# Optimization experiments

Measured on AMD Instinct MI355X. Metric: run time of the kernel, lower is better.

Reference implementation:

```python
import jax, jax.numpy as jnp
import numpy as np

B, T, C, H = 8, 1024, 1024, 16
HD = C // H  # head dim = 64
NEG = -1e9


def setup_inputs() -> dict:
    key = jax.random.key(0)
    ks = jax.random.split(key, 10)
    total = B * T
    x = jax.random.normal(ks[0], (total, C), dtype=jnp.float32)
    # identity pack: each padded row is a contiguous chunk of tokens
    padpack_index = jnp.arange(total, dtype=jnp.int64).reshape(B, T)
    # sorted per-row sequence ids -> block-diagonal attention within each packed row
    padpack_batch = jnp.sort(jax.random.randint(ks[1], (B, T), 0, 4, dtype=jnp.int32), axis=-1)
    padpack_inverse_index = jnp.arange(total, dtype=jnp.int64)
    s = 1.0 / np.sqrt(C)
    Wq = jax.random.uniform(ks[2], (C, C), jnp.float32, -s, s)
    bq = jax.random.uniform(ks[3], (C,), jnp.float32, -s, s)
    Wk = jax.random.uniform(ks[4], (C, C), jnp.float32, -s, s)
    bk = jax.random.uniform(ks[5], (C,), jnp.float32, -s, s)
    Wv = jax.random.uniform(ks[6], (C, C), jnp.float32, -s, s)
    bv = jax.random.uniform(ks[7], (C,), jnp.float32, -s, s)
    Wp = jax.random.uniform(ks[8], (C, C), jnp.float32, -s, s)
    bp = jax.random.uniform(ks[9], (C,), jnp.float32, -s, s)
    return {"x": x, "padpack_index": padpack_index, "padpack_batch": padpack_batch,
            "padpack_inverse_index": padpack_inverse_index,
            "Wq": Wq, "bq": bq, "Wk": Wk, "bk": bk, "Wv": Wv, "bv": bv, "Wp": Wp, "bp": bp}


def reference(x, padpack_index, padpack_batch, padpack_inverse_index,
              Wq, bq, Wk, bk, Wv, bv, Wp, bp):
    # gather ragged tokens into padded [B, T, C]
    xp = x[padpack_index]
    # torch Linear: y = x @ W.T + b
    q = (xp @ Wq.T + bq).reshape(B, T, H, HD)
    k = (xp @ Wk.T + bk).reshape(B, T, H, HD)
    v = (xp @ Wv.T + bv).reshape(B, T, H, HD)
    scale = 1.0 / np.sqrt(HD).astype(np.float32)
    att = jnp.einsum('bihd,bjhd->bhij', q, k) * scale  # [B,H,T,T]
    # mask: token pairs from different packed sequences cannot attend
    mask = (padpack_batch[:, :, None] != padpack_batch[:, None, :])[:, None]  # [B,1,T,T]
    att = jnp.where(mask, NEG, att)
    att = jax.nn.softmax(att, axis=-1)
    y = jnp.einsum('bhij,bjhd->bihd', att, v).reshape(B, T, C)
    y = y @ Wp.T + bp
    # scatter back to ragged layout [total_tokens, C]
    return y.reshape(B * T, C)[padpack_inverse_index]
```

## Files before the change

### kernel.cpp

```cpp
#include <hip/hip_runtime.h>


typedef __attribute__((ext_vector_type(8))) short short8;
typedef __attribute__((ext_vector_type(4))) float f32x4;

#define MFMA16(a, b, c) __builtin_amdgcn_mfma_f32_16x16x32_bf16((a), (b), (c), 0, 0, 0)

__device__ __forceinline__ ushort f2b(float f) {
  union { float f; unsigned u; } v; v.f = f;
  unsigned u = v.u;
  return (ushort)((u + 0x7fffu + ((u >> 16) & 1u)) >> 16);
}

__device__ __forceinline__ void gload16(const void* g, void* l) {
  __builtin_amdgcn_global_load_lds((const __attribute__((address_space(1))) unsigned int*)g,
                                   (__attribute__((address_space(3))) unsigned int*)l,
                                   16, 0, 0);
}

__device__ __forceinline__ void cvt4(const float* __restrict__ s, ushort* __restrict__ d) {
  const float4 v = *(const float4*)s;
  ushort4 r; r.x = f2b(v.x); r.y = f2b(v.y); r.z = f2b(v.z); r.w = f2b(v.w);
  *(ushort4*)d = r;
}

__global__ __launch_bounds__(256) void prep(const float* __restrict__ x,
    const float* __restrict__ wq, const float* __restrict__ wk,
    const float* __restrict__ wv, const float* __restrict__ wp,
    ushort* __restrict__ xb, ushort* __restrict__ wb) {
  const long long e0 = ((long long)blockIdx.x * 256 + threadIdx.x) * 4;
  const long long NX = 8388608ll;
  if (e0 < NX) {
    cvt4(x + e0, xb + e0);
  } else {
    const long long t = e0 - NX;
    const int sel = (int)(t >> 20);
    const float* w = sel == 0 ? wq : sel == 1 ? wk : sel == 2 ? wv : wp;
    cvt4(w + (t & 1048575), wb + t);
  }
}

__global__ void seg_bounds(const int* __restrict__ pb, int* __restrict__ bnd) {
  const int b = blockIdx.x, i = threadIdx.x;
  const int* p = pb + b * 1024;
  const int cur = p[i];
  const int prev = (i == 0) ? -1 : p[i - 1];
  for (int v = prev + 1; v <= cur; ++v) bnd[b * 8 + v] = i;
  if (i == 1023)
    for (int v = cur + 1; v <= 4; ++v) bnd[b * 8 + v] = 1024;
}

__global__ __launch_bounds__(256) void gemm_qkv(const ushort* __restrict__ X,
    const ushort* __restrict__ Wq, const ushort* __restrict__ Wk, const ushort* __restrict__ Wv,
    const float* __restrict__ bq, const float* __restrict__ bk, const float* __restrict__ bv,
    ushort* __restrict__ Qb, ushort* __restrict__ Kb, ushort* __restrict__ Vt) {
  __shared__ __align__(16) char smem[33792];
  ushort (*As)[32] = (ushort(*)[32])smem;
  ushort (*Bs)[32] = (ushort(*)[32])(smem + 8192);

  const int z = blockIdx.z;
  const ushort* W = (z == 0) ? Wq : (z == 1) ? Wk : Wv;
  const float* bias = (z == 0) ? bq : (z == 1) ? bk : bv;

  const int tid = threadIdx.x;
  const int lane = tid & 63, wv4 = tid >> 6;
  const int wr = wv4 >> 1, wc = wv4 & 1;
  const int lg = lane >> 4, lc = lane & 15;
  const int m0 = blockIdx.y * 128, n0 = blockIdx.x * 128;

  f32x4 acc[4][4] = {};

  const ushort* ga = X + (size_t)(m0 + (tid >> 2)) * 1024 + (tid & 3) * 8;
  const ushort* gb = W + (size_t)(n0 + (tid >> 2)) * 1024 + (tid & 3) * 8;
  char* la = smem + tid * 16;
  char* lb = smem + 8192 + tid * 16;

  for (int k0 = 0; k0 < 1024; k0 += 32) {
    gload16(ga + k0, la);
    gload16(ga + k0 + 64 * 1024, la + 4096);
    gload16(gb + k0, lb);
    gload16(gb + k0 + 64 * 1024, lb + 4096);
    __syncthreads();
    short8 af[4], bfr[4];
#pragma unroll
    for (int m = 0; m < 4; ++m) af[m] = *(const short8*)&As[wr * 64 + m * 16 + lc][lg * 8];
#pragma unroll
    for (int n = 0; n < 4; ++n) bfr[n] = *(const short8*)&Bs[wc * 64 + n * 16 + lc][lg * 8];
#pragma unroll
    for (int m = 0; m < 4; ++m)
#pragma unroll
      for (int n = 0; n < 4; ++n)
        acc[m][n] = MFMA16(af[m], bfr[n], acc[m][n]);
    __syncthreads();
  }

  float bval[4];
#pragma unroll
  for (int n = 0; n < 4; ++n) bval[n] = bias[n0 + wc * 64 + n * 16 + lc];

  if (z < 2) {
    ushort* dst = z ? Kb : Qb;
#pragma unroll
    for (int m = 0; m < 4; ++m)
#pragma unroll
      for (int j = 0; j < 4; ++j) {
        const size_t row = m0 + wr * 64 + m * 16 + lg * 4 + j;
#pragma unroll
        for (int n = 0; n < 4; ++n)
          dst[row * 1024 + n0 + wc * 64 + n * 16 + lc] = f2b(acc[m][n][j] + bval[n]);
      }
  } else {
    ushort (*Ts)[132] = (ushort(*)[132])smem;
#pragma unroll
    for (int m = 0; m < 4; ++m)
#pragma unroll
      for (int n = 0; n < 4; ++n)
#pragma unroll
        for (int j = 0; j < 4; ++j)
          Ts[wr * 64 + m * 16 + lg * 4 + j][wc * 64 + n * 16 + lc] = f2b(acc[m][n][j] + bval[n]);
    __syncthreads();
    const int c = tid >> 1;
    const int th = (tid & 1) * 64;
    const int gc = n0 + c;
    const int gt = m0 + th;
    const int b = gt >> 10, t = gt & 1023;
    ushort* dp = Vt + ((size_t)((b * 16 + (gc >> 6)) * 64 + (gc & 63))) * 1024 + t;
#pragma unroll
    for (int g = 0; g < 8; ++g) {
      short8 pk;
#pragma unroll
      for (int u = 0; u < 8; ++u) pk[u] = (short)Ts[th + g * 8 + u][c];
      *(short8*)(dp + g * 8) = pk;
    }
  }
}

__global__ __launch_bounds__(256) void attn(const ushort* __restrict__ Q,
    const ushort* __restrict__ K, const ushort* __restrict__ Vt,
    const int* __restrict__ bnd, ushort* __restrict__ O) {
  __shared__ __align__(16) char kvbuf[2][16384];
  __shared__ __align__(16) ushort Plds[4][16][68];

  const int tid = threadIdx.x, lane = tid & 63, w = tid >> 6;
  const int lg = lane >> 4, lc = lane & 15;

  const int id = blockIdx.x;
  const int xcd = id & 7, slot = id >> 3;
  const int bh = xcd + 8 * (slot >> 4), qt = slot & 15;
  const int b = bh >> 4, h = bh & 15;
  const int q0 = qt * 64 + w * 16;

  const int* bd = bnd + b * 8;
  const int b1 = bd[1], b2 = bd[2], b3 = bd[3], b4 = bd[4];
#define SEGID(k) (((k) >= b1) + ((k) >= b2) + ((k) >= b3) + ((k) >= b4))

  const int qid = SEGID(q0 + lc);
  int klo_l = (qid > 0) ? b1 : 0;
  klo_l = (qid > 1) ? b2 : klo_l;
  klo_l = (qid > 2) ? b3 : klo_l;
  int khi_l = (qid > 0) ? b2 : b1;
  khi_l = (qid > 1) ? b3 : khi_l;
  khi_l = (qid > 2) ? b4 : khi_l;

  const int bq_lo = SEGID(qt * 64), bq_hi = SEGID(qt * 64 + 63);
  unsigned am = 0;
#pragma unroll
  for (int jt = 0; jt < 16; ++jt) {
    const int tlo = SEGID(jt * 64), thi = SEGID(jt * 64 + 63);
    if (thi >= bq_lo && tlo <= bq_hi) am |= (1u << jt);
  }

  const ushort* qp = Q + (size_t)(b * 1024 + q0 + lc) * 1024 + h * 64 + lg * 8;
  const short8 qf0 = *(const short8*)qp;
  const short8 qf1 = *(const short8*)(qp + 32);

  const int r0 = tid >> 3;
  const int c16 = (tid & 7) ^ (r0 & 7);
  const ushort* Kg0 = K + (size_t)(b * 1024 + r0) * 1024 + h * 64 + c16 * 8;
  const ushort* Kg1 = Kg0 + (size_t)32 * 1024;
  const ushort* Vg0 = Vt + (size_t)(bh * 64 + r0) * 1024 + c16 * 8;
  const ushort* Vg1 = Vg0 + (size_t)32 * 1024;

#define STAGE(bufp, j) { \
    gload16(Kg0 + (size_t)(j) * 1024, (bufp) + tid * 16); \
    gload16(Kg1 + (size_t)(j) * 1024, (bufp) + 4096 + tid * 16); \
    gload16(Vg0 + (j), (bufp) + 8192 + tid * 16); \
    gload16(Vg1 + (j), (bufp) + 12288 + tid * 16); }

#define SOFF(r, ch) ((r) * 128 + ((((ch) ^ ((r) & 7))) << 4))

  float mr = -1e30f, lr = 0.f;
  f32x4 o[4] = {};

  unsigned rem = am;
  int jc = __builtin_ctz(rem) * 64;
  rem &= rem - 1;
  STAGE(kvbuf[0], jc)
  __syncthreads();
  int cur = 0;

  for (;;) {
    int jn = -1;
    if (rem) {
      jn = __builtin_ctz(rem) * 64;
      rem &= rem - 1;
      STAGE(kvbuf[cur ^ 1], jn)
    }
    const char* bufK = kvbuf[cur];
    const char* bufV = kvbuf[cur] + 8192;

    short8 kf[8];
#pragma unroll
    for (int n = 0; n < 4; ++n) {
      const int rr = n * 16 + lc;
      kf[2 * n] = *(const short8*)(bufK + SOFF(rr, lg));
      kf[2 * n + 1] = *(const short8*)(bufK + SOFF(rr, lg + 4));
    }
    f32x4 s[4];
    __builtin_amdgcn_s_setprio(1);
#pragma unroll
    for (int n = 0; n < 4; ++n) {
      f32x4 z = {};
      z = MFMA16(kf[2 * n], qf0, z);
      s[n] = MFMA16(kf[2 * n + 1], qf1, z);
    }
    __builtin_amdgcn_s_setprio(0);

#pragma unroll
    for (int n = 0; n < 4; ++n) {
      const int kk = jc + n * 16 + lg * 4;
#pragma unroll
      for (int r = 0; r < 4; ++r) {
        const bool ok = (kk + r >= klo_l) && (kk + r < khi_l);
        s[n][r] = ok ? s[n][r] * 0.125f : -1e9f;
      }
    }

    float rm = fmaxf(fmaxf(fmaxf(s[0][0], s[0][1]), fmaxf(s[0][2], s[0][3])),
                     fmaxf(fmaxf(fmaxf(s[1][0], s[1][1]), fmaxf(s[1][2], s[1][3])),
                           fmaxf(fmaxf(fmaxf(s[2][0], s[2][1]), fmaxf(s[2][2], s[2][3])),
                                 fmaxf(fmaxf(s[3][0], s[3][1]), fmaxf(s[3][2], s[3][3])))));
    rm = fmaxf(rm, __shfl_xor(rm, 16));
    rm = fmaxf(rm, __shfl_xor(rm, 32));
    float mn = mr;
    if (!__all(rm <= mr + 8.f)) {
      mn = fmaxf(mr, rm);
      const float sf = __expf(mr - mn);
      mr = mn;
      lr *= sf;
      const float s0 = __shfl(sf, lg * 4 + 0);
      const float s1 = __shfl(sf, lg * 4 + 1);
      const float s2 = __shfl(sf, lg * 4 + 2);
      const float s3 = __shfl(sf, lg * 4 + 3);
#pragma unroll
      for (int n = 0; n < 4; ++n) {
        o[n][0] *= s0; o[n][1] *= s1; o[n][2] *= s2; o[n][3] *= s3;
      }
    }
    float rs = 0.f;
#pragma unroll
    for (int n = 0; n < 4; ++n)
#pragma unroll
      for (int r = 0; r < 4; ++r) {
        const float p = __expf(s[n][r] - mn);
        s[n][r] = p; rs += p;
      }
    rs += __shfl_xor(rs, 16);
    rs += __shfl_xor(rs, 32);
    lr += rs;

#pragma unroll
    for (int n = 0; n < 4; ++n) {
      ushort4 pk;
      pk.x = f2b(s[n][0]); pk.y = f2b(s[n][1]); pk.z = f2b(s[n][2]); pk.w = f2b(s[n][3]);
      *(ushort4*)&Plds[w][lc][n * 16 + lg * 4] = pk;
    }
    asm volatile("s_waitcnt lgkmcnt(0)" ::: "memory");
    __builtin_amdgcn_sched_barrier(0);
    const short8 p0 = *(const short8*)&Plds[w][lc][lg * 8];
    const short8 p1 = *(const short8*)&Plds[w][lc][32 + lg * 8];
    __builtin_amdgcn_sched_barrier(0);

    short8 vv[8];
#pragma unroll
    for (int n = 0; n < 4; ++n) {
      const int rr = n * 16 + lc;
      vv[2 * n] = *(const short8*)(bufV + SOFF(rr, lg));
      vv[2 * n + 1] = *(const short8*)(bufV + SOFF(rr, lg + 4));
    }
    __builtin_amdgcn_s_setprio(1);
#pragma unroll
    for (int n = 0; n < 4; ++n) {
      o[n] = MFMA16(p0, vv[2 * n], o[n]);
      o[n] = MFMA16(p1, vv[2 * n + 1], o[n]);
    }
    __builtin_amdgcn_s_setprio(0);

    if (jn < 0) break;
    __syncthreads();
    cur ^= 1;
    jc = jn;
  }

  const float linv = 1.f / lr;
  const float i0 = __shfl(linv, lg * 4 + 0);
  const float i1 = __shfl(linv, lg * 4 + 1);
  const float i2 = __shfl(linv, lg * 4 + 2);
  const float i3 = __shfl(linv, lg * 4 + 3);
#pragma unroll
  for (int n = 0; n < 4; ++n) {
    const size_t base = (size_t)(b * 1024 + q0) * 1024 + h * 64 + n * 16 + lc;
    O[base + 0 * 1024 + (size_t)lg * 4096] = f2b(o[n][0] * i0);
    O[base + 1 * 1024 + (size_t)lg * 4096] = f2b(o[n][1] * i1);
    O[base + 2 * 1024 + (size_t)lg * 4096] = f2b(o[n][2] * i2);
    O[base + 3 * 1024 + (size_t)lg * 4096] = f2b(o[n][3] * i3);
  }
#undef STAGE
#undef SOFF
#undef SEGID
}

__global__ __launch_bounds__(256) void gemm_proj(const ushort* __restrict__ X,
    const ushort* __restrict__ W, const float* __restrict__ bias, float* __restrict__ out) {
  __shared__ __align__(16) char smem[16384];
  ushort (*As)[32] = (ushort(*)[32])smem;
  ushort (*Bs)[32] = (ushort(*)[32])(smem + 8192);
  const int tid = threadIdx.x;
  const int lane = tid & 63, wv4 = tid >> 6;
  const int wr = wv4 >> 1, wc = wv4 & 1;
  const int lg = lane >> 4, lc = lane & 15;
  const int m0 = blockIdx.y * 128, n0 = blockIdx.x * 128;
  f32x4 acc[4][4] = {};
  const ushort* ga = X + (size_t)(m0 + (tid >> 2)) * 1024 + (tid & 3) * 8;
  const ushort* gb = W + (size_t)(n0 + (tid >> 2)) * 1024 + (tid & 3) * 8;
  char* la = smem + tid * 16;
  char* lb = smem + 8192 + tid * 16;
  for (int k0 = 0; k0 < 1024; k0 += 32) {
    gload16(ga + k0, la);
    gload16(ga + k0 + 64 * 1024, la + 4096);
    gload16(gb + k0, lb);
    gload16(gb + k0 + 64 * 1024, lb + 4096);
    __syncthreads();
    short8 af[4], bfr[4];
#pragma unroll
    for (int m = 0; m < 4; ++m) af[m] = *(const short8*)&As[wr * 64 + m * 16 + lc][lg * 8];
#pragma unroll
    for (int n = 0; n < 4; ++n) bfr[n] = *(const short8*)&Bs[wc * 64 + n * 16 + lc][lg * 8];
#pragma unroll
    for (int m = 0; m < 4; ++m)
#pragma unroll
      for (int n = 0; n < 4; ++n)
        acc[m][n] = MFMA16(af[m], bfr[n], acc[m][n]);
    __syncthreads();
  }
  float bval[4];
#pragma unroll
  for (int n = 0; n < 4; ++n) bval[n] = bias[n0 + wc * 64 + n * 16 + lc];
#pragma unroll
  for (int m = 0; m < 4; ++m)
#pragma unroll
    for (int j = 0; j < 4; ++j) {
      const size_t row = m0 + wr * 64 + m * 16 + lg * 4 + j;
#pragma unroll
      for (int n = 0; n < 4; ++n)
        out[row * 1024 + n0 + wc * 64 + n * 16 + lc] = acc[m][n][j] + bval[n];
    }
}

extern "C" void kernel_launch(void* const* d_in, const int* in_sizes, int n_in,
                              void* d_out, int out_size, void* d_ws, size_t ws_size,
                              hipStream_t stream) {
  const float* x  = (const float*)d_in[0];
  const int*  pb  = (const int*)d_in[2];
  const float* Wq = (const float*)d_in[4]; const float* bq = (const float*)d_in[5];
  const float* Wk = (const float*)d_in[6]; const float* bk = (const float*)d_in[7];
  const float* Wv = (const float*)d_in[8]; const float* bv = (const float*)d_in[9];
  const float* Wp = (const float*)d_in[10]; const float* bp = (const float*)d_in[11];
  float* out = (float*)d_out;
  char* ws = (char*)d_ws;

  ushort* xb = (ushort*)ws;
  ushort* wb = (ushort*)(ws + (16u << 20));
  ushort* Qb = (ushort*)(ws + (24u << 20));
  ushort* Kb = (ushort*)(ws + (40u << 20));
  ushort* Vt = (ushort*)(ws + (56u << 20));
  int*    bnd = (int*)(ws + (72u << 20));
  ushort* Ob = xb;

  prep<<<12288, 256, 0, stream>>>(x, Wq, Wk, Wv, Wp, xb, wb);
  seg_bounds<<<8, 1024, 0, stream>>>(pb, bnd);
  gemm_qkv<<<dim3(8, 64, 3), 256, 0, stream>>>(xb, wb, wb + (1 << 20), wb + (2 << 20),
                                               bq, bk, bv, Qb, Kb, Vt);
  attn<<<2048, 256, 0, stream>>>(Qb, Kb, Vt, bnd, Ob);
  gemm_proj<<<dim3(8, 64), 256, 0, stream>>>(Ob, wb + (3 << 20), bp, out);
}
```

Before: 177.1 us.

## Deepen GEMM K-tile to 64 with XOR-swizzled LDS and XCD-aware block mapping

```diff
diff --git a/kernel.cpp b/kernel.cpp
--- a/kernel.cpp
+++ b/kernel.cpp
@@ -51,55 +51,72 @@
 }
 
 __global__ __launch_bounds__(256) void gemm_qkv(const ushort* __restrict__ X,
-    const ushort* __restrict__ Wq, const ushort* __restrict__ Wk, const ushort* __restrict__ Wv,
+    const ushort* __restrict__ Wc,
     const float* __restrict__ bq, const float* __restrict__ bk, const float* __restrict__ bv,
     ushort* __restrict__ Qb, ushort* __restrict__ Kb, ushort* __restrict__ Vt) {
   __shared__ __align__(16) char smem[33792];
-  ushort (*As)[32] = (ushort(*)[32])smem;
-  ushort (*Bs)[32] = (ushort(*)[32])(smem + 8192);
-
-  const int z = blockIdx.z;
-  const ushort* W = (z == 0) ? Wq : (z == 1) ? Wk : Wv;
-  const float* bias = (z == 0) ? bq : (z == 1) ? bk : bv;
 
   const int tid = threadIdx.x;
   const int lane = tid & 63, wv4 = tid >> 6;
   const int wr = wv4 >> 1, wc = wv4 & 1;
   const int lg = lane >> 4, lc = lane & 15;
-  const int m0 = blockIdx.y * 128, n0 = blockIdx.x * 128;
+
+  const int id = blockIdx.x;
+  const int xcd = id & 7, slot = id >> 3;
+  const int m0 = (xcd * 8 + (slot & 7)) << 7;
+  const int n0 = (slot >> 3) << 7;
+  const int sel = n0 >> 10, nloc = n0 & 1023;
 
   f32x4 acc[4][4] = {};
 
-  const ushort* ga = X + (size_t)(m0 + (tid >> 2)) * 1024 + (tid & 3) * 8;
-  const ushort* gb = W + (size_t)(n0 + (tid >> 2)) * 1024 + (tid & 3) * 8;
+  const int r0 = tid >> 3;
+  const int csrc = (tid & 7) ^ (r0 & 7);
+  const ushort* ga = X + (size_t)(m0 + r0) * 1024 + csrc * 8;
+  const ushort* gb = Wc + (size_t)(n0 + r0) * 1024 + csrc * 8;
   char* la = smem + tid * 16;
-  char* lb = smem + 8192 + tid * 16;
-
-  for (int k0 = 0; k0 < 1024; k0 += 32) {
-    gload16(ga + k0, la);
-    gload16(ga + k0 + 64 * 1024, la + 4096);
-    gload16(gb + k0, lb);
-    gload16(gb + k0 + 64 * 1024, lb + 4096);
-    __syncthreads();
-    short8 af[4], bfr[4];
-#pragma unroll
-    for (int m = 0; m < 4; ++m) af[m] = *(const short8*)&As[wr * 64 + m * 16 + lc][lg * 8];
-#pragma unroll
-    for (int n = 0; n < 4; ++n) bfr[n] = *(const short8*)&Bs[wc * 64 + n * 16 + lc][lg * 8];
+  char* lb = smem + 16384 + tid * 16;
+  const int cA0 = (lg ^ (lc & 7)) << 4;
+  const int cA1 = ((4 + lg) ^ (lc & 7)) << 4;
+
+  for (int k0 = 0; k0 < 1024; k0 += 64) {
+#pragma unroll
+    for (int j = 0; j < 4; ++j) {
+      gload16(ga + k0 + (size_t)j * 32 * 1024, la + j * 4096);
+      gload16(gb + k0 + (size_t)j * 32 * 1024, lb + j * 4096);
+    }
+    __syncthreads();
+    short8 af[4][2], bf[4][2];
+#pragma unroll
+    for (int m = 0; m < 4; ++m) {
+      const char* rp = smem + (wr * 64 + m * 16 + lc) * 128;
+      af[m][0] = *(const short8*)(rp + cA0);
+      af[m][1] = *(const short8*)(rp + cA1);
+    }
+#pragma unroll
+    for (int n = 0; n < 4; ++n) {
+      const char* rp = smem + 16384 + (wc * 64 + n * 16 + lc) * 128;
+      bf[n][0] = *(const short8*)(rp + cA0);
+      bf[n][1] = *(const short8*)(rp + cA1);
+    }
+    __builtin_amdgcn_s_setprio(1);
 #pragma unroll
     for (int m = 0; m < 4; ++m)
 #pragma unroll
-      for (int n = 0; n < 4; ++n)
-        acc[m][n] = MFMA16(af[m], bfr[n], acc[m][n]);
-    __syncthreads();
-  }
-
+      for (int n = 0; n < 4; ++n) {
+        acc[m][n] = MFMA16(af[m][0], bf[n][0], acc[m][n]);
+        acc[m][n] = MFMA16(af[m][1], bf[n][1], acc[m][n]);
+      }
+    __builtin_amdgcn_s_setprio(0);
+    __syncthreads();
+  }
+
+  const float* bias = sel == 0 ? bq : sel == 1 ? bk : bv;
   float bval[4];
 #pragma unroll
-  for (int n = 0; n < 4; ++n) bval[n] = bias[n0 + wc * 64 + n * 16 + lc];
-
-  if (z < 2) {
-    ushort* dst = z ? Kb : Qb;
+  for (int n = 0; n < 4; ++n) bval[n] = bias[nloc + wc * 64 + n * 16 + lc];
+
+  if (sel < 2) {
+    ushort* dst = sel ? Kb : Qb;
 #pragma unroll
     for (int m = 0; m < 4; ++m)
 #pragma unroll
@@ -107,7 +124,7 @@
         const size_t row = m0 + wr * 64 + m * 16 + lg * 4 + j;
 #pragma unroll
         for (int n = 0; n < 4; ++n)
-          dst[row * 1024 + n0 + wc * 64 + n * 16 + lc] = f2b(acc[m][n][j] + bval[n]);
+          dst[row * 1024 + nloc + wc * 64 + n * 16 + lc] = f2b(acc[m][n][j] + bval[n]);
       }
   } else {
     ushort (*Ts)[132] = (ushort(*)[132])smem;
@@ -121,7 +138,7 @@
     __syncthreads();
     const int c = tid >> 1;
     const int th = (tid & 1) * 64;
-    const int gc = n0 + c;
+    const int gc = nloc + c;
     const int gt = m0 + th;
     const int b = gt >> 10, t = gt & 1023;
     ushort* dp = Vt + ((size_t)((b * 16 + (gc >> 6)) * 64 + (gc & 63))) * 1024 + t;
@@ -322,37 +339,60 @@
 
 __global__ __launch_bounds__(256) void gemm_proj(const ushort* __restrict__ X,
     const ushort* __restrict__ W, const float* __restrict__ bias, float* __restrict__ out) {
-  __shared__ __align__(16) char smem[16384];
-  ushort (*As)[32] = (ushort(*)[32])smem;
-  ushort (*Bs)[32] = (ushort(*)[32])(smem + 8192);
+  __shared__ __align__(16) char smem[32768];
   const int tid = threadIdx.x;
   const int lane = tid & 63, wv4 = tid >> 6;
   const int wr = wv4 >> 1, wc = wv4 & 1;
   const int lg = lane >> 4, lc = lane & 15;
-  const int m0 = blockIdx.y * 128, n0 = blockIdx.x * 128;
+
+  const int id = blockIdx.x;
+  const int xcd = id & 7, slot = id >> 3;
+  const int m0 = (xcd * 8 + (slot & 7)) << 7;
+  const int n0 = (slot >> 3) << 7;
+
   f32x4 acc[4][4] = {};
-  const ushort* ga = X + (size_t)(m0 + (tid >> 2)) * 1024 + (tid & 3) * 8;
-  const ushort* gb = W + (size_t)(n0 + (tid >> 2)) * 1024 + (tid & 3) * 8;
+
+  const int r0 = tid >> 3;
+  const int csrc = (tid & 7) ^ (r0 & 7);
+  const ushort* ga = X + (size_t)(m0 + r0) * 1024 + csrc * 8;
+  const ushort* gb = W + (size_t)(n0 + r0) * 1024 + csrc * 8;
   char* la = smem + tid * 16;
-  char* lb = smem + 8192 + tid * 16;
-  for (int k0 = 0; k0 < 1024; k0 += 32) {
-    gload16(ga + k0, la);
-    gload16(ga + k0 + 64 * 1024, la + 4096);
-    gload16(gb + k0, lb);
-    gload16(gb + k0 + 64 * 1024, lb + 4096);
-    __syncthreads();
-    short8 af[4], bfr[4];
-#pragma unroll
-    for (int m = 0; m < 4; ++m) af[m] = *(const short8*)&As[wr * 64 + m * 16 + lc][lg * 8];
-#pragma unroll
-    for (int n = 0; n < 4; ++n) bfr[n] = *(const short8*)&Bs[wc * 64 + n * 16 + lc][lg * 8];
+  char* lb = smem + 16384 + tid * 16;
+  const int cA0 = (lg ^ (lc & 7)) << 4;
+  const int cA1 = ((4 + lg) ^ (lc & 7)) << 4;
+
+  for (int k0 = 0; k0 < 1024; k0 += 64) {
+#pragma unroll
+    for (int j = 0; j < 4; ++j) {
+      gload16(ga + k0 + (size_t)j * 32 * 1024, la + j * 4096);
+      gload16(gb + k0 + (size_t)j * 32 * 1024, lb + j * 4096);
+    }
+    __syncthreads();
+    short8 af[4][2], bf[4][2];
+#pragma unroll
+    for (int m = 0; m < 4; ++m) {
+      const char* rp = smem + (wr * 64 + m * 16 + lc) * 128;
+      af[m][0] = *(const short8*)(rp + cA0);
+      af[m][1] = *(const short8*)(rp + cA1);
+    }
+#pragma unroll
+    for (int n = 0; n < 4; ++n) {
+      const char* rp = smem + 16384 + (wc * 64 + n * 16 + lc) * 128;
+      bf[n][0] = *(const short8*)(rp + cA0);
+      bf[n][1] = *(const short8*)(rp + cA1);
+    }
+    __builtin_amdgcn_s_setprio(1);
 #pragma unroll
     for (int m = 0; m < 4; ++m)
 #pragma unroll
-      for (int n = 0; n < 4; ++n)
-        acc[m][n] = MFMA16(af[m], bfr[n], acc[m][n]);
-    __syncthreads();
-  }
+      for (int n = 0; n < 4; ++n) {
+        acc[m][n] = MFMA16(af[m][0], bf[n][0], acc[m][n]);
+        acc[m][n] = MFMA16(af[m][1], bf[n][1], acc[m][n]);
+      }
+    __builtin_amdgcn_s_setprio(0);
+    __syncthreads();
+  }
+
   float bval[4];
 #pragma unroll
   for (int n = 0; n < 4; ++n) bval[n] = bias[n0 + wc * 64 + n * 16 + lc];
@@ -389,8 +429,7 @@
 
   prep<<<12288, 256, 0, stream>>>(x, Wq, Wk, Wv, Wp, xb, wb);
   seg_bounds<<<8, 1024, 0, stream>>>(pb, bnd);
-  gemm_qkv<<<dim3(8, 64, 3), 256, 0, stream>>>(xb, wb, wb + (1 << 20), wb + (2 << 20),
-                                               bq, bk, bv, Qb, Kb, Vt);
+  gemm_qkv<<<1536, 256, 0, stream>>>(xb, wb, bq, bk, bv, Qb, Kb, Vt);
   attn<<<2048, 256, 0, stream>>>(Qb, Kb, Vt, bnd, Ob);
-  gemm_proj<<<dim3(8, 64), 256, 0, stream>>>(Ob, wb + (3 << 20), bp, out);
-}
+  gemm_proj<<<512, 256, 0, stream>>>(Ob, wb + (3 << 20), bp, out);
+}
```

Result: faster. 155.7 us (-12.1%).

## Replace QKV and projection GEMMs with double-buffered 256-row templated GEMM

Applied to the files above, without the earlier changes.

```diff
diff --git a/kernel.cpp b/kernel.cpp
--- a/kernel.cpp
+++ b/kernel.cpp
@@ -50,89 +50,165 @@
     for (int v = cur + 1; v <= 4; ++v) bnd[b * 8 + v] = 1024;
 }
 
-__global__ __launch_bounds__(256) void gemm_qkv(const ushort* __restrict__ X,
-    const ushort* __restrict__ Wq, const ushort* __restrict__ Wk, const ushort* __restrict__ Wv,
-    const float* __restrict__ bq, const float* __restrict__ bk, const float* __restrict__ bv,
-    ushort* __restrict__ Qb, ushort* __restrict__ Kb, ushort* __restrict__ Vt) {
-  __shared__ __align__(16) char smem[33792];
-  ushort (*As)[32] = (ushort(*)[32])smem;
-  ushort (*Bs)[32] = (ushort(*)[32])(smem + 8192);
-
-  const int z = blockIdx.z;
-  const ushort* W = (z == 0) ? Wq : (z == 1) ? Wk : Wv;
-  const float* bias = (z == 0) ? bq : (z == 1) ? bk : bv;
-
-  const int tid = threadIdx.x;
-  const int lane = tid & 63, wv4 = tid >> 6;
-  const int wr = wv4 >> 1, wc = wv4 & 1;
+template <int BN, int WM, int WN, int MODE>
+__global__ __launch_bounds__(512, 2) void gemm8(
+    const ushort* __restrict__ A, const ushort* __restrict__ Bw,
+    const float* __restrict__ bias0, const float* __restrict__ bias1,
+    const float* __restrict__ bias2,
+    ushort* __restrict__ O0, ushort* __restrict__ O1, ushort* __restrict__ O2,
+    float* __restrict__ Of) {
+  constexpr int BM = 256;
+  constexpr int MREP = BM / (WM * 16);
+  constexpr int NREP = BN / (WN * 16);
+  constexpr int ACH = BM * 64;
+  constexpr int BCH = BN * 64;
+  constexpr int GLA = ACH / 8192;
+  constexpr int GLB = BCH / 8192;
+  constexpr int GL = GLA + GLB;
+  constexpr int BUFB = 2 * (ACH + BCH);
+  __shared__ __align__(16) char smem[2 * BUFB];
+
+  const int tid = threadIdx.x, lane = tid & 63, wid = tid >> 6;
+  const int wr = wid / WN, wc = wid % WN;
   const int lg = lane >> 4, lc = lane & 15;
-  const int m0 = blockIdx.y * 128, n0 = blockIdx.x * 128;
-
-  f32x4 acc[4][4] = {};
-
-  const ushort* ga = X + (size_t)(m0 + (tid >> 2)) * 1024 + (tid & 3) * 8;
-  const ushort* gb = W + (size_t)(n0 + (tid >> 2)) * 1024 + (tid & 3) * 8;
-  char* la = smem + tid * 16;
-  char* lb = smem + 8192 + tid * 16;
-
-  for (int k0 = 0; k0 < 1024; k0 += 32) {
-    gload16(ga + k0, la);
-    gload16(ga + k0 + 64 * 1024, la + 4096);
-    gload16(gb + k0, lb);
-    gload16(gb + k0 + 64 * 1024, lb + 4096);
-    __syncthreads();
-    short8 af[4], bfr[4];
-#pragma unroll
-    for (int m = 0; m < 4; ++m) af[m] = *(const short8*)&As[wr * 64 + m * 16 + lc][lg * 8];
-#pragma unroll
-    for (int n = 0; n < 4; ++n) bfr[n] = *(const short8*)&Bs[wc * 64 + n * 16 + lc][lg * 8];
-#pragma unroll
-    for (int m = 0; m < 4; ++m)
-#pragma unroll
-      for (int n = 0; n < 4; ++n)
-        acc[m][n] = MFMA16(af[m], bfr[n], acc[m][n]);
-    __syncthreads();
-  }
-
-  float bval[4];
-#pragma unroll
-  for (int n = 0; n < 4; ++n) bval[n] = bias[n0 + wc * 64 + n * 16 + lc];
-
-  if (z < 2) {
-    ushort* dst = z ? Kb : Qb;
-#pragma unroll
-    for (int m = 0; m < 4; ++m)
+
+  const int id = blockIdx.x;
+  const int s = id >> 3;
+  const int m0 = ((id & 7) * 4 + (s & 3)) << 8;
+  const int n0 = (s >> 2) * BN;
+
+  f32x4 acc[MREP][NREP] = {};
+
+  const int sr0 = tid >> 2;
+  const int sc0 = (tid & 3) ^ (sr0 & 3);
+
+#define STAGE_PAIR(p, kh, kt) { \
+    char* ad = smem + (p) * BUFB + (kh) * ACH; \
+    char* bd = smem + (p) * BUFB + 2 * ACH + (kh) * BCH; \
+    const int kcol = (kt) * 64 + (kh) * 32; \
+    gload16(A + (size_t)(m0 + sr0) * 1024 + kcol + sc0 * 8, ad + tid * 16); \
+    if constexpr (GLA == 2) \
+      gload16(A + (size_t)(m0 + 128 + sr0) * 1024 + kcol + sc0 * 8, ad + (tid + 512) * 16); \
+    gload16(Bw + (size_t)(n0 + sr0) * 1024 + kcol + sc0 * 8, bd + tid * 16); \
+    if constexpr (GLB == 2) \
+      gload16(Bw + (size_t)(n0 + 128 + sr0) * 1024 + kcol + sc0 * 8, bd + (tid + 512) * 16); \
+  }
+
+#define PHASE_COMPUTE(p, kh) { \
+    const char* ab = smem + (p) * BUFB + (kh) * ACH; \
+    const char* bb = smem + (p) * BUFB + 2 * ACH + (kh) * BCH; \
+    short8 af[MREP]; short8 bf[NREP]; \
+    _Pragma("unroll") \
+    for (int f = 0; f < MREP; ++f) { \
+      const int row = wr * (MREP * 16) + f * 16 + lc; \
+      af[f] = *(const short8*)(ab + row * 64 + ((lg ^ (row & 3)) << 4)); \
+    } \
+    _Pragma("unroll") \
+    for (int g = 0; g < NREP; ++g) { \
+      const int row = wc * (NREP * 16) + g * 16 + lc; \
+      bf[g] = *(const short8*)(bb + row * 64 + ((lg ^ (row & 3)) << 4)); \
+    } \
+    asm volatile("s_waitcnt lgkmcnt(0)" ::: "memory"); \
+    __builtin_amdgcn_sched_barrier(0); \
+    __builtin_amdgcn_s_setprio(1); \
+    _Pragma("unroll") \
+    for (int f = 0; f < MREP; ++f) \
+      _Pragma("unroll") \
+      for (int g = 0; g < NREP; ++g) \
+        acc[f][g] = MFMA16(af[f], bf[g], acc[f][g]); \
+    __builtin_amdgcn_s_setprio(0); \
+  }
+
+#define WAIT_VM_GL() { \
+    if constexpr (GL == 4) asm volatile("s_waitcnt vmcnt(4)" ::: "memory"); \
+    else asm volatile("s_waitcnt vmcnt(3)" ::: "memory"); }
+
+  STAGE_PAIR(0, 0, 0)
+  STAGE_PAIR(0, 1, 0)
+
+#pragma unroll 2
+  for (int i = 0; i < 30; ++i) {
+    const int t = i >> 1, kh = i & 1, p = t & 1;
+    WAIT_VM_GL()
+    __builtin_amdgcn_s_barrier();
+    __builtin_amdgcn_sched_barrier(0);
+    STAGE_PAIR(p ^ 1, kh, t + 1)
+    PHASE_COMPUTE(p, kh)
+  }
+  WAIT_VM_GL()
+  __builtin_amdgcn_s_barrier();
+  __builtin_amdgcn_sched_barrier(0);
+  PHASE_COMPUTE(1, 0)
+  asm volatile("s_waitcnt vmcnt(0)" ::: "memory");
+  __builtin_amdgcn_s_barrier();
+  __builtin_amdgcn_sched_barrier(0);
+  PHASE_COMPUTE(1, 1)
+
+  if constexpr (MODE == 0) {
+    const int sel = n0 >> 10, nloc = n0 & 1023;
+    const float* bias = sel == 0 ? bias0 : sel == 1 ? bias1 : bias2;
+    float bval[NREP];
+#pragma unroll
+    for (int g = 0; g < NREP; ++g) bval[g] = bias[nloc + wc * (NREP * 16) + g * 16 + lc];
+    if (sel < 2) {
+      ushort* dst = sel ? O1 : O0;
+#pragma unroll
+      for (int f = 0; f < MREP; ++f)
+#pragma unroll
+        for (int j = 0; j < 4; ++j) {
+          const size_t row = m0 + wr * (MREP * 16) + f * 16 + lg * 4 + j;
+#pragma unroll
+          for (int g = 0; g < NREP; ++g)
+            dst[row * 1024 + nloc + wc * (NREP * 16) + g * 16 + lc] =
+                f2b(acc[f][g][j] + bval[g]);
+        }
+    } else {
+      ushort (*Ts)[264] = (ushort(*)[264])smem;
+#pragma unroll
+      for (int mh = 0; mh < 2; ++mh) {
+        __syncthreads();
+        if (wr == mh) {
+#pragma unroll
+          for (int f = 0; f < MREP; ++f)
+#pragma unroll
+            for (int g = 0; g < NREP; ++g)
+#pragma unroll
+              for (int j = 0; j < 4; ++j)
+                Ts[f * 16 + lg * 4 + j][wc * (NREP * 16) + g * 16 + lc] =
+                    f2b(acc[f][g][j] + bval[g]);
+        }
+        __syncthreads();
+        const int c = tid >> 1, th = (tid & 1) * 64;
+        const int gt = m0 + mh * 128;
+        const int b = gt >> 10, t0 = (gt & 1023) + th;
+        const int gc = nloc + c;
+        ushort* dp = O2 + ((size_t)((b * 16 + (gc >> 6)) * 64 + (gc & 63))) * 1024 + t0;
+#pragma unroll
+        for (int gb = 0; gb < 8; ++gb) {
+          short8 pk;
+#pragma unroll
+          for (int u = 0; u < 8; ++u) pk[u] = (short)Ts[th + gb * 8 + u][c];
+          *(short8*)(dp + gb * 8) = pk;
+        }
+      }
+    }
+  } else {
+    float bval[NREP];
+#pragma unroll
+    for (int g = 0; g < NREP; ++g) bval[g] = bias0[n0 + wc * (NREP * 16) + g * 16 + lc];
+#pragma unroll
+    for (int f = 0; f < MREP; ++f)
 #pragma unroll
       for (int j = 0; j < 4; ++j) {
-        const size_t row = m0 + wr * 64 + m * 16 + lg * 4 + j;
-#pragma unroll
-        for (int n = 0; n < 4; ++n)
-          dst[row * 1024 + n0 + wc * 64 + n * 16 + lc] = f2b(acc[m][n][j] + bval[n]);
+        const size_t row = m0 + wr * (MREP * 16) + f * 16 + lg * 4 + j;
+#pragma unroll
+        for (int g = 0; g < NREP; ++g)
+          Of[row * 1024 + n0 + wc * (NREP * 16) + g * 16 + lc] = acc[f][g][j] + bval[g];
       }
-  } else {
-    ushort (*Ts)[132] = (ushort(*)[132])smem;
-#pragma unroll
-    for (int m = 0; m < 4; ++m)
-#pragma unroll
-      for (int n = 0; n < 4; ++n)
-#pragma unroll
-        for (int j = 0; j < 4; ++j)
-          Ts[wr * 64 + m * 16 + lg * 4 + j][wc * 64 + n * 16 + lc] = f2b(acc[m][n][j] + bval[n]);
-    __syncthreads();
-    const int c = tid >> 1;
-    const int th = (tid & 1) * 64;
-    const int gc = n0 + c;
-    const int gt = m0 + th;
-    const int b = gt >> 10, t = gt & 1023;
-    ushort* dp = Vt + ((size_t)((b * 16 + (gc >> 6)) * 64 + (gc & 63))) * 1024 + t;
-#pragma unroll
-    for (int g = 0; g < 8; ++g) {
-      short8 pk;
-#pragma unroll
-      for (int u = 0; u < 8; ++u) pk[u] = (short)Ts[th + g * 8 + u][c];
-      *(short8*)(dp + g * 8) = pk;
-    }
-  }
+  }
+#undef STAGE_PAIR
+#undef PHASE_COMPUTE
+#undef WAIT_VM_GL
 }
 
 __global__ __launch_bounds__(256) void attn(const ushort* __restrict__ Q,
@@ -320,53 +396,6 @@
 #undef SEGID
 }
 
-__global__ __launch_bounds__(256) void gemm_proj(const ushort* __restrict__ X,
-    const ushort* __restrict__ W, const float* __restrict__ bias, float* __restrict__ out) {
-  __shared__ __align__(16) char smem[16384];
-  ushort (*As)[32] = (ushort(*)[32])smem;
-  ushort (*Bs)[32] = (ushort(*)[32])(smem + 8192);
-  const int tid = threadIdx.x;
-  const int lane = tid & 63, wv4 = tid >> 6;
-  const int wr = wv4 >> 1, wc = wv4 & 1;
-  const int lg = lane >> 4, lc = lane & 15;
-  const int m0 = blockIdx.y * 128, n0 = blockIdx.x * 128;
-  f32x4 acc[4][4] = {};
-  const ushort* ga = X + (size_t)(m0 + (tid >> 2)) * 1024 + (tid & 3) * 8;
-  const ushort* gb = W + (size_t)(n0 + (tid >> 2)) * 1024 + (tid & 3) * 8;
-  char* la = smem + tid * 16;
-  char* lb = smem + 8192 + tid * 16;
-  for (int k0 = 0; k0 < 1024; k0 += 32) {
-    gload16(ga + k0, la);
-    gload16(ga + k0 + 64 * 1024, la + 4096);
-    gload16(gb + k0, lb);
-    gload16(gb + k0 + 64 * 1024, lb + 4096);
-    __syncthreads();
-    short8 af[4], bfr[4];
-#pragma unroll
-    for (int m = 0; m < 4; ++m) af[m] = *(const short8*)&As[wr * 64 + m * 16 + lc][lg * 8];
-#pragma unroll
-    for (int n = 0; n < 4; ++n) bfr[n] = *(const short8*)&Bs[wc * 64 + n * 16 + lc][lg * 8];
-#pragma unroll
-    for (int m = 0; m < 4; ++m)
-#pragma unroll
-      for (int n = 0; n < 4; ++n)
-        acc[m][n] = MFMA16(af[m], bfr[n], acc[m][n]);
-    __syncthreads();
-  }
-  float bval[4];
-#pragma unroll
-  for (int n = 0; n < 4; ++n) bval[n] = bias[n0 + wc * 64 + n * 16 + lc];
-#pragma unroll
-  for (int m = 0; m < 4; ++m)
-#pragma unroll
-    for (int j = 0; j < 4; ++j) {
-      const size_t row = m0 + wr * 64 + m * 16 + lg * 4 + j;
-#pragma unroll
-      for (int n = 0; n < 4; ++n)
-        out[row * 1024 + n0 + wc * 64 + n * 16 + lc] = acc[m][n][j] + bval[n];
-    }
-}
-
 extern "C" void kernel_launch(void* const* d_in, const int* in_sizes, int n_in,
                               void* d_out, int out_size, void* d_ws, size_t ws_size,
                               hipStream_t stream) {
@@ -389,8 +418,8 @@
 
   prep<<<12288, 256, 0, stream>>>(x, Wq, Wk, Wv, Wp, xb, wb);
   seg_bounds<<<8, 1024, 0, stream>>>(pb, bnd);
-  gemm_qkv<<<dim3(8, 64, 3), 256, 0, stream>>>(xb, wb, wb + (1 << 20), wb + (2 << 20),
-                                               bq, bk, bv, Qb, Kb, Vt);
+  gemm8<256, 2, 4, 0><<<384, 512, 0, stream>>>(xb, wb, bq, bk, bv, Qb, Kb, Vt, nullptr);
   attn<<<2048, 256, 0, stream>>>(Qb, Kb, Vt, bnd, Ob);
-  gemm_proj<<<dim3(8, 64), 256, 0, stream>>>(Ob, wb + (3 << 20), bp, out);
-}
+  gemm8<128, 4, 2, 1><<<256, 512, 0, stream>>>(Ob, wb + (3 << 20), bp,
+                                               nullptr, nullptr, nullptr, nullptr, nullptr, out);
+}
```

New measurement: 159.3 us. -10.1%, faster.
